# Optimization experiments

Hardware: AMD Instinct MI355X
Metric: run time of the kernel (lower is better)

## Reference

```python
import jax, jax.numpy as jnp
import numpy as np

N_NODES = 100000
N_DIM = 128   # node feature dim
L10 = 128
L11 = 128     # dim_hop0 == L11 (required by Spatial_Attention_0 einsum)
B = 2048      # batch of target nodes
S1 = 10       # hop-1 fanout
S2 = 25       # hop-2 fanout per hop-1 neighbor


def setup_inputs() -> dict:
    key = jax.random.key(0)
    ks = jax.random.split(key, 9)
    tn = lambda k, shape: jax.random.truncated_normal(k, -2.0, 2.0, shape, jnp.float32) * 0.1 - 0.1
    return {
        "x": jax.random.normal(ks[0], (N_NODES, N_DIM), jnp.float32),
        "samples": jax.random.randint(ks[1], (B, 1 + S1 + S1 * S2), 0, N_NODES),
        "V1_h1_att": tn(ks[2], (L11, N_DIM)),
        "w1_h1": tn(ks[3], (2 * L11,)),
        "V1_h0_att": tn(ks[4], (L10, L11)),
        "w1_h0": tn(ks[5], (2 * L10,)),
        "V1_h1": tn(ks[6], (L11, N_DIM)),
        "V1_h0": tn(ks[7], (L10, L11)),
        "W_hops": tn(ks[8], (L11, 2 * L11)),
    }


def _att1(feat, V, w):
    # feat: [..., s, 2*n]; project both halves with V [L, n], score with w [2L],
    # leaky_relu then softmax over the neighbor axis (axis -2 of feat).
    n = V.shape[1]
    L = V.shape[0]
    t1 = jnp.einsum('...sn,ln->...sl', feat[..., :n], V)
    t2 = jnp.einsum('...sn,ln->...sl', feat[..., n:], V)
    logits = jnp.einsum('l,...sl->...s', w[:L], t1) + jnp.einsum('l,...sl->...s', w[L:], t2)
    return jax.nn.softmax(jax.nn.leaky_relu(logits), axis=-1)


def reference(x, samples, V1_h1_att, w1_h1, V1_h0_att, w1_h0, V1_h1, V1_h0, W_hops):
    s1, s2 = S1, S2
    idx2 = samples[:, -(s1 * s2):].reshape(-1, s1, s2)   # hop-2 neighbor ids [B,s1,s2]
    idx1 = samples[:, 1:1 + s1]                          # hop-1 neighbor ids [B,s1]
    idx0 = samples[:, 0]                                 # targets [B]

    # ---- hop-1 aggregation (attention over the s2 hop-2 neighbors) ----
    fea_n2 = x[idx2]                                     # [B,s1,s2,n] irregular gather
    fea_t1 = x[idx1]                                     # [B,s1,n]
    fea_tar2 = jnp.concatenate(
        [jnp.broadcast_to(fea_t1[:, :, None, :], fea_n2.shape), fea_n2], axis=-1)
    beta1 = _att1(fea_tar2, V1_h1_att, w1_h1)            # [B,s1,s2]
    emb_n2 = jnp.einsum('bstn,ln->bstl', fea_n2, V1_h1)  # [B,s1,s2,L11]
    agg1 = jnp.einsum('bst,bstl->bsl', beta1, emb_n2)    # [B,s1,L11]
    emb_t1 = jnp.einsum('bsn,ln->bsl', fea_t1, V1_h1)    # [B,s1,L11]
    hop1 = jax.nn.sigmoid(
        jnp.einsum('dj,bsj->bsd', W_hops, jnp.concatenate([emb_t1, agg1], -1)))  # [B,s1,L11]

    # ---- hop-0 aggregation (attention over the s1 hop-1 neighbors) ----
    fea_t0 = x[idx0]                                     # [B,n]
    fea_tar1 = jnp.concatenate(
        [jnp.broadcast_to(fea_t0[:, None, :], fea_t1.shape), fea_t1], axis=-1)
    beta0 = _att1(fea_tar1, V1_h1_att, w1_h1)            # [B,s1]
    agg0 = jnp.einsum('bs,bsl->bl', beta0, emb_t1)       # emb of hop-1 nbrs == emb_t1
    emb_t0 = fea_t0 @ V1_h1.T                            # [B,L11]
    hop0 = jax.nn.sigmoid(jnp.concatenate([emb_t0, agg0], -1) @ W_hops.T)  # [B,L11]

    # ---- combine hops with Spatial_Attention_0 ----
    t1c = jnp.einsum('bd,ld->bl', hop0, V1_h0_att)       # target proj (tiled over s1)
    t2c = jnp.einsum('bsd,ld->bsl', hop1, V1_h0_att)     # [B,s1,L10]
    logits = (jnp.einsum('l,bl->b', w1_h0[:L10], t1c)[:, None]
              + jnp.einsum('l,bsl->bs', w1_h0[L10:], t2c))
    beta_h = jax.nn.softmax(jax.nn.leaky_relu(logits), axis=1)  # [B,s1]
    emb_h1 = jnp.einsum('bsd,ld->bsl', hop1, V1_h0)      # [B,s1,L10]
    fea_out = jnp.einsum('bs,bsl->bl', beta_h, emb_h1)   # [B,L10]

    beta_step = jnp.concatenate([beta_h[:, :, None], beta1], axis=2)  # [B,s1,1+s2]
    return fea_out.T, beta_step
```

## Files before the change

kernel.cpp:

```cpp
#include <hip/hip_runtime.h>
#include <math.h>

#define S1C 10
#define S2C 25
#define DC 128
#define NSAMP 261
#define NBATCH 2048
#define FEA_SZ (128*2048)

#define WS_BPK   512
#define WS_V0T   (WS_BPK + 16384)
#define WS_AGGF  (WS_V0T + 16384)

typedef float f32x4 __attribute__((ext_vector_type(4)));
typedef short s16x8 __attribute__((ext_vector_type(8)));

__device__ __forceinline__ float lrelu(float v) { return v > 0.f ? v : 0.01f * v; }
__device__ __forceinline__ float sigm(float v) { return 1.f / (1.f + __expf(-v)); }
__device__ __forceinline__ float dot4(float4 a, float4 b) {
    return a.x * b.x + a.y * b.y + a.z * b.z + a.w * b.w;
}
__device__ __forceinline__ unsigned short f2bf(float f) {
    unsigned u = __float_as_uint(f);
    unsigned r = (u + 0x7FFFu + ((u >> 16) & 1u)) >> 16;
    return (unsigned short)r;
}

__global__ void prep_all_kernel(const float* __restrict__ Vh1a, const float* __restrict__ w1,
                                const float* __restrict__ Vh0a, const float* __restrict__ w0,
                                const float* __restrict__ V1h1, const float* __restrict__ Whops,
                                const float* __restrict__ V1h0, float* __restrict__ ws) {
    const int blk = blockIdx.x, tid = threadIdx.x;
    if (blk == 0) {
        for (int o = tid; o < 512; o += 256) {
            int which = o >> 7, n = o & 127;
            const float* V = (which < 2) ? Vh1a : Vh0a;
            const float* w = (which < 2) ? w1 : w0;
            int off = (which & 1) * 128;
            float acc = 0.f;
            for (int l = 0; l < 128; ++l) acc += V[l * 128 + n] * w[off + l];
            ws[o] = acc;
        }
    } else if (blk <= 128) {
        int e = (blk - 1) * 256 + tid;
        int j  = e & 7;
        int l  = (e >> 3) & 63;
        int kb = (e >> 9) & 7;
        int nt = (e >> 12) & 7;
        int d  = nt * 16 + (l & 15);
        int k  = kb * 32 + ((l >> 4) & 3) * 8 + j;
        int which = k >> 7, kk = k & 127;
        float acc = 0.f;
        for (int jj = 0; jj < 128; ++jj)
            acc += Whops[(size_t)d * 256 + which * 128 + jj] * V1h1[(size_t)jj * 128 + kk];
        unsigned short* bpk = (unsigned short*)(ws + WS_BPK);
        bpk[e] = f2bf(acc);
    } else {
        int dd = (blk - 129) * 2 + (tid >> 7);
        int l = tid & 127;
        ws[WS_V0T + (size_t)dd * 128 + l] = V1h0[(size_t)l * 128 + dd];
    }
}

__global__ __launch_bounds__(256) void nbr_kernel(
    const float* __restrict__ x, const int* __restrict__ samples,
    const float* __restrict__ ws, unsigned short* __restrict__ aggF,
    float* __restrict__ out)
{
    const int s = blockIdx.x, b = blockIdx.y;
    const int tid = threadIdx.x, g = tid >> 5, lane = tid & 31;

    __shared__ __align__(16) float sNbr[25][132];
    __shared__ float sD[26];
    __shared__ float sBeta[25];

    float4 a1v = *(const float4*)(ws + lane * 4);
    float4 a2v = *(const float4*)(ws + 128 + lane * 4);
    const int* sidx = samples + (size_t)b * NSAMP;

    const bool has3 = (g < 2);
    int n0 = sidx[11 + s * S2C + g];
    int n1 = sidx[11 + s * S2C + 8 + g];
    int n2 = sidx[11 + s * S2C + 16 + g];
    int n3 = has3 ? ((g == 0) ? sidx[11 + s * S2C + 24] : sidx[1 + s]) : 0;

    float4 v0 = *(const float4*)(x + (size_t)n0 * DC + lane * 4);
    float4 v1 = *(const float4*)(x + (size_t)n1 * DC + lane * 4);
    float4 v2 = *(const float4*)(x + (size_t)n2 * DC + lane * 4);
    float4 v3 = make_float4(0.f, 0.f, 0.f, 0.f);
    if (has3) v3 = *(const float4*)(x + (size_t)n3 * DC + lane * 4);

    *(float4*)(&sNbr[g][lane * 4]) = v0;
    *(float4*)(&sNbr[8 + g][lane * 4]) = v1;
    *(float4*)(&sNbr[16 + g][lane * 4]) = v2;
    if (g == 0) *(float4*)(&sNbr[24][lane * 4]) = v3;

    float p0 = dot4(v0, a2v);
    float p1 = dot4(v1, a2v);
    float p2 = dot4(v2, a2v);
    float p3 = has3 ? dot4(v3, (g == 0) ? a2v : a1v) : 0.f;
    #pragma unroll
    for (int o = 16; o > 0; o >>= 1) {
        p0 += __shfl_xor(p0, o, 32);
        p1 += __shfl_xor(p1, o, 32);
        p2 += __shfl_xor(p2, o, 32);
        p3 += __shfl_xor(p3, o, 32);
    }
    if (lane == 0) {
        sD[g] = p0; sD[8 + g] = p1; sD[16 + g] = p2;
        if (has3) sD[24 + g] = p3;
    }
    __syncthreads();

    if (tid < 32) {
        float c1 = sD[25];
        float v = (lane < 25) ? lrelu(c1 + sD[lane]) : -3.4e38f;
        float m = v;
        for (int o = 16; o > 0; o >>= 1) m = fmaxf(m, __shfl_xor(m, o, 32));
        float e = (lane < 25) ? __expf(v - m) : 0.f;
        float ssum = e;
        for (int o = 16; o > 0; o >>= 1) ssum += __shfl_xor(ssum, o, 32);
        if (lane < 25) {
            float bt = e / ssum;
            sBeta[lane] = bt;
            out[FEA_SZ + (size_t)b * 260 + s * 26 + 1 + lane] = bt;
        }
    }
    __syncthreads();

    if (tid < 128) {
        float acc = 0.f;
        #pragma unroll
        for (int t = 0; t < 25; ++t) acc += sBeta[t] * sNbr[t][tid];
        aggF[((size_t)b * 10 + s) * 128 + tid] = f2bf(acc);
    }
}

__global__ __launch_bounds__(256, 4) void hopfused_kernel(
    const float* __restrict__ x, const int* __restrict__ samples,
    const float* __restrict__ ws, const unsigned short* __restrict__ aggF,
    float* __restrict__ out)
{
    const int b0 = blockIdx.x * 2;
    const int tid = threadIdx.x;
    const int w = tid >> 6;
    const int lane = tid & 63;
    const int lg16 = lane >> 4;
    const int l15 = lane & 15;

    __shared__ __align__(16) float sX[22][128];
    __shared__ __align__(16) short sXb[32][264];
    __shared__ float sLgP[4][32];
    __shared__ __align__(16) float sHopH[2][128];
    __shared__ float sD[22];
    __shared__ float sBeta0[2][10];
    __shared__ float sBH[2][10];
    __shared__ int sNode[22];

    if (tid < 22) {
        int bb = tid / 11, s = tid - bb * 11;
        sNode[tid] = (s < 10) ? samples[(size_t)(b0 + bb) * NSAMP + 1 + s]
                              : samples[(size_t)(b0 + bb) * NSAMP];
    }
    for (int i = tid; i < 330; i += 256) {
        int rr = i / 33, c8 = i - rr * 33;
        int row = (rr < 5) ? 11 + rr : 22 + rr;
        s16x8 z = (s16x8)(short)0;
        *(s16x8*)(&sXb[row][c8 * 8]) = z;
    }
    __syncthreads();

    for (int i = tid; i < 22 * 32; i += 256) {
        int row = i >> 5, seg = i & 31;
        *(float4*)(&sX[row][seg * 4]) =
            *(const float4*)(x + (size_t)sNode[row] * DC + seg * 4);
    }
    for (int i = tid; i < 320; i += 256) {
        int row20 = i >> 4, seg = i & 15;
        int bb = row20 / 10, s = row20 - bb * 10;
        *(s16x8*)(&sXb[bb * 16 + s][128 + seg * 8]) =
            *(const s16x8*)(aggF + ((size_t)(b0 + bb) * 10 + s) * 128 + seg * 8);
    }
    __syncthreads();

    {
        int gg = tid >> 5, ln = tid & 31;
        for (int rd = 0, r = gg; rd < 3; ++rd, r += 8) {
            float p = 0.f;
            if (r < 22) {
                int s = (r < 11) ? r : r - 11;
                const float* av = ws + ((s < 10) ? 128 : 0);
                float4 v = *(const float4*)(&sX[r][ln * 4]);
                float4 a = *(const float4*)(av + ln * 4);
                p = dot4(v, a);
            }
            for (int o = 16; o > 0; o >>= 1) p += __shfl_xor(p, o, 32);
            if (r < 22 && ln == 0) sD[r] = p;
        }
    }
    __syncthreads();

    if (tid < 32) {
        int bb = tid >> 4, j = tid & 15;
        float cc = sD[bb * 11 + 10];
        float v = (j < 10) ? lrelu(cc + sD[bb * 11 + j]) : -3.4e38f;
        float m = v;
        for (int o = 8; o > 0; o >>= 1) m = fmaxf(m, __shfl_xor(m, o, 16));
        float e = (j < 10) ? __expf(v - m) : 0.f;
        float ss = e;
        for (int o = 8; o > 0; o >>= 1) ss += __shfl_xor(ss, o, 16);
        if (j < 10) sBeta0[bb][j] = e / ss;
    }
    __syncthreads();

    {
        int bb = tid >> 7, n = tid & 127;
        float acc = 0.f;
        #pragma unroll
        for (int s = 0; s < 10; ++s) acc += sBeta0[bb][s] * sX[bb * 11 + s][n];
        sXb[bb * 16 + 10][128 + n] = (short)f2bf(acc);
    }
    for (int i = tid; i < 22 * 128; i += 256) {
        int m = i >> 7, k = i & 127;
        int row = (m < 11) ? m : m + 5;
        sXb[row][k] = (short)f2bf(sX[m][k]);
    }
    __syncthreads();

    const unsigned short* bpk = (const unsigned short*)(ws + WS_BPK);
    const int nt0 = 2 * w, nt1 = nt0 + 1;
    f32x4 acc00 = {0.f, 0.f, 0.f, 0.f}, acc01 = {0.f, 0.f, 0.f, 0.f};
    f32x4 acc10 = {0.f, 0.f, 0.f, 0.f}, acc11 = {0.f, 0.f, 0.f, 0.f};
    #pragma unroll
    for (int kb = 0; kb < 8; ++kb) {
        s16x8 a0 = *(const s16x8*)(&sXb[l15][kb * 32 + lg16 * 8]);
        s16x8 a1 = *(const s16x8*)(&sXb[16 + l15][kb * 32 + lg16 * 8]);
        s16x8 bw0 = *(const s16x8*)(bpk + ((size_t)(nt0 * 8 + kb) * 64 + lane) * 8);
        s16x8 bw1 = *(const s16x8*)(bpk + ((size_t)(nt1 * 8 + kb) * 64 + lane) * 8);
        acc00 = __builtin_amdgcn_mfma_f32_16x16x32_bf16(a0, bw0, acc00, 0, 0, 0);
        acc01 = __builtin_amdgcn_mfma_f32_16x16x32_bf16(a0, bw1, acc01, 0, 0, 0);
        acc10 = __builtin_amdgcn_mfma_f32_16x16x32_bf16(a1, bw0, acc10, 0, 0, 0);
        acc11 = __builtin_amdgcn_mfma_f32_16x16x32_bf16(a1, bw1, acc11, 0, 0, 0);
    }

    float h00[4], h01[4], h10[4], h11[4];
    #pragma unroll
    for (int r = 0; r < 4; ++r) {
        h00[r] = sigm(acc00[r]); h01[r] = sigm(acc01[r]);
        h10[r] = sigm(acc10[r]); h11[r] = sigm(acc11[r]);
    }

    const int c0 = nt0 * 16 + l15, c1 = nt1 * 16 + l15;
    const float b1c0 = ws[256 + c0], b1c1 = ws[256 + c1];
    const float b2c0 = ws[384 + c0], b2c1 = ws[384 + c1];
    #pragma unroll
    for (int mt = 0; mt < 2; ++mt) {
        #pragma unroll
        for (int r = 0; r < 4; ++r) {
            int s = lg16 * 4 + r;
            float ha = mt ? h10[r] : h00[r];
            float hb = mt ? h11[r] : h01[r];
            float p;
            if (s < 10)       p = ha * b2c0 + hb * b2c1;
            else if (s == 10) p = ha * b1c0 + hb * b1c1;
            else              p = 0.f;
            #pragma unroll
            for (int o = 1; o < 16; o <<= 1) p += __shfl_xor(p, o, 64);
            if (l15 == 0) sLgP[w][mt * 16 + s] = p;
        }
    }
    __syncthreads();

    if (tid < 32) {
        int bb = tid >> 4, j = tid & 15;
        float lgj = 0.f, lg10 = 0.f;
        #pragma unroll
        for (int wv = 0; wv < 4; ++wv) {
            lgj  += sLgP[wv][bb * 16 + j];
            lg10 += sLgP[wv][bb * 16 + 10];
        }
        float v = (j < 10) ? lrelu(lg10 + lgj) : -3.4e38f;
        float m = v;
        for (int o = 8; o > 0; o >>= 1) m = fmaxf(m, __shfl_xor(m, o, 16));
        float e = (j < 10) ? __expf(v - m) : 0.f;
        float ss = e;
        for (int o = 8; o > 0; o >>= 1) ss += __shfl_xor(ss, o, 16);
        if (j < 10) {
            float bh = e / ss;
            sBH[bb][j] = bh;
            out[FEA_SZ + (size_t)(b0 + bb) * 260 + j * 26] = bh;
        }
    }
    __syncthreads();

    #pragma unroll
    for (int bb = 0; bb < 2; ++bb) {
        float p0 = 0.f, p1 = 0.f;
        #pragma unroll
        for (int r = 0; r < 4; ++r) {
            int s = lg16 * 4 + r;
            if (s < 10) {
                float bh = sBH[bb][s];
                p0 += bh * (bb ? h10[r] : h00[r]);
                p1 += bh * (bb ? h11[r] : h01[r]);
            }
        }
        p0 += __shfl_xor(p0, 16, 64); p0 += __shfl_xor(p0, 32, 64);
        p1 += __shfl_xor(p1, 16, 64); p1 += __shfl_xor(p1, 32, 64);
        if (lg16 == 0) {
            sHopH[bb][nt0 * 16 + l15] = p0;
            sHopH[bb][nt1 * 16 + l15] = p1;
        }
    }
    __syncthreads();

    {
        const float* v0t = ws + WS_V0T;
        int c = tid & 127, bb = tid >> 7;
        float acc2 = 0.f;
        for (int dd = 0; dd < 128; dd += 4) {
            float4 hh = *(const float4*)(&sHopH[bb][dd]);
            acc2 += hh.x * v0t[(size_t)(dd + 0) * 128 + c]
                  + hh.y * v0t[(size_t)(dd + 1) * 128 + c]
                  + hh.z * v0t[(size_t)(dd + 2) * 128 + c]
                  + hh.w * v0t[(size_t)(dd + 3) * 128 + c];
        }
        out[(size_t)c * 2048 + b0 + bb] = acc2;
    }
}

extern "C" void kernel_launch(void* const* d_in, const int* in_sizes, int n_in,
                              void* d_out, int out_size, void* d_ws, size_t ws_size,
                              hipStream_t stream) {
    const float* x      = (const float*)d_in[0];
    const int*   samples= (const int*)d_in[1];
    const float* V1h1a  = (const float*)d_in[2];
    const float* w1h1   = (const float*)d_in[3];
    const float* V1h0a  = (const float*)d_in[4];
    const float* w1h0   = (const float*)d_in[5];
    const float* V1h1   = (const float*)d_in[6];
    const float* V1h0   = (const float*)d_in[7];
    const float* Whops  = (const float*)d_in[8];
    float* outp = (float*)d_out;
    float* ws   = (float*)d_ws;
    unsigned short* aggF = (unsigned short*)(ws + WS_AGGF);

    hipLaunchKernelGGL(prep_all_kernel, dim3(193), dim3(256), 0, stream,
                       V1h1a, w1h1, V1h0a, w1h0, V1h1, Whops, V1h0, ws);
    hipLaunchKernelGGL(nbr_kernel, dim3(10, 2048), dim3(256), 0, stream,
                       x, samples, ws, aggF, outp);
    hipLaunchKernelGGL(hopfused_kernel, dim3(1024), dim3(256), 0, stream,
                       x, samples, ws, aggF, outp);
}
```

Before: 71.79 us.

## Convert node features to bf16 once per call and gather bf16 rows

Adds a pass in the prep kernel that converts the full feature table to bf16 in workspace. New neighbor and hop kernels then gather bf16 rows instead of fp32, halving the bytes of the irregular gathers. In exchange it streams the whole table each call and loses precision in the attention inputs. The new path is enabled only when the workspace is large enough.

```diff
diff --git a/kernel.cpp b/kernel.cpp
--- a/kernel.cpp
+++ b/kernel.cpp
@@ -6,14 +6,18 @@
 #define DC 128
 #define NSAMP 261
 #define NBATCH 2048
+#define N_NODES 100000
 #define FEA_SZ (128*2048)
 
 #define WS_BPK   512
 #define WS_V0T   (WS_BPK + 16384)
 #define WS_AGGF  (WS_V0T + 16384)
+#define WS_XB    (WS_AGGF + 1310720)
+#define WS_END   (WS_XB + 6400000)
 
 typedef float f32x4 __attribute__((ext_vector_type(4)));
 typedef short s16x8 __attribute__((ext_vector_type(8)));
+typedef short s16x4 __attribute__((ext_vector_type(4)));
 
 __device__ __forceinline__ float lrelu(float v) { return v > 0.f ? v : 0.01f * v; }
 __device__ __forceinline__ float sigm(float v) { return 1.f / (1.f + __expf(-v)); }
@@ -25,11 +29,15 @@
     unsigned r = (u + 0x7FFFu + ((u >> 16) & 1u)) >> 16;
     return (unsigned short)r;
 }
+__device__ __forceinline__ float bf2f(unsigned short us) {
+    return __uint_as_float(((unsigned)us) << 16);
+}
 
 __global__ void prep_all_kernel(const float* __restrict__ Vh1a, const float* __restrict__ w1,
                                 const float* __restrict__ Vh0a, const float* __restrict__ w0,
                                 const float* __restrict__ V1h1, const float* __restrict__ Whops,
-                                const float* __restrict__ V1h0, float* __restrict__ ws) {
+                                const float* __restrict__ V1h0, const float* __restrict__ x,
+                                unsigned short* __restrict__ xb, float* __restrict__ ws) {
     const int blk = blockIdx.x, tid = threadIdx.x;
     if (blk == 0) {
         for (int o = tid; o < 512; o += 256) {
@@ -55,12 +63,289 @@
             acc += Whops[(size_t)d * 256 + which * 128 + jj] * V1h1[(size_t)jj * 128 + kk];
         unsigned short* bpk = (unsigned short*)(ws + WS_BPK);
         bpk[e] = f2bf(acc);
-    } else {
+    } else if (blk <= 192) {
         int dd = (blk - 129) * 2 + (tid >> 7);
         int l = tid & 127;
         ws[WS_V0T + (size_t)dd * 128 + l] = V1h0[(size_t)l * 128 + dd];
-    }
-}
+    } else {
+        const int total4 = N_NODES * DC / 4;
+        const int stride = (gridDim.x - 193) * 256;
+        const float4* x4 = (const float4*)x;
+        for (int i = (blk - 193) * 256 + tid; i < total4; i += stride) {
+            float4 v = x4[i];
+            s16x4 o;
+            o[0] = (short)f2bf(v.x); o[1] = (short)f2bf(v.y);
+            o[2] = (short)f2bf(v.z); o[3] = (short)f2bf(v.w);
+            *(s16x4*)(xb + (size_t)i * 4) = o;
+        }
+    }
+}
+
+
+__global__ __launch_bounds__(256) void nbr_b_kernel(
+    const unsigned short* __restrict__ xb, const int* __restrict__ samples,
+    const float* __restrict__ ws, unsigned short* __restrict__ aggF,
+    float* __restrict__ out)
+{
+    const int s = blockIdx.x, b = blockIdx.y;
+    const int tid = threadIdx.x, g = tid >> 5, lane = tid & 31;
+
+    __shared__ __align__(16) unsigned short sNbr[25][136];
+    __shared__ float sD[26];
+    __shared__ float sBeta[25];
+
+    float4 a1v = *(const float4*)(ws + lane * 4);
+    float4 a2v = *(const float4*)(ws + 128 + lane * 4);
+    const int* sidx = samples + (size_t)b * NSAMP;
+
+    const bool has3 = (g < 2);
+    int n0 = sidx[11 + s * S2C + g];
+    int n1 = sidx[11 + s * S2C + 8 + g];
+    int n2 = sidx[11 + s * S2C + 16 + g];
+    int n3 = has3 ? ((g == 0) ? sidx[11 + s * S2C + 24] : sidx[1 + s]) : 0;
+
+    s16x4 v0 = *(const s16x4*)(xb + (size_t)n0 * DC + lane * 4);
+    s16x4 v1 = *(const s16x4*)(xb + (size_t)n1 * DC + lane * 4);
+    s16x4 v2 = *(const s16x4*)(xb + (size_t)n2 * DC + lane * 4);
+    s16x4 v3 = (s16x4)(short)0;
+    if (has3) v3 = *(const s16x4*)(xb + (size_t)n3 * DC + lane * 4);
+
+    *(s16x4*)(&sNbr[g][lane * 4]) = v0;
+    *(s16x4*)(&sNbr[8 + g][lane * 4]) = v1;
+    *(s16x4*)(&sNbr[16 + g][lane * 4]) = v2;
+    if (g == 0) *(s16x4*)(&sNbr[24][lane * 4]) = v3;
+
+    float p0 = bf2f((unsigned short)v0[0]) * a2v.x + bf2f((unsigned short)v0[1]) * a2v.y
+             + bf2f((unsigned short)v0[2]) * a2v.z + bf2f((unsigned short)v0[3]) * a2v.w;
+    float p1 = bf2f((unsigned short)v1[0]) * a2v.x + bf2f((unsigned short)v1[1]) * a2v.y
+             + bf2f((unsigned short)v1[2]) * a2v.z + bf2f((unsigned short)v1[3]) * a2v.w;
+    float p2 = bf2f((unsigned short)v2[0]) * a2v.x + bf2f((unsigned short)v2[1]) * a2v.y
+             + bf2f((unsigned short)v2[2]) * a2v.z + bf2f((unsigned short)v2[3]) * a2v.w;
+    float4 av3 = (g == 0) ? a2v : a1v;
+    float p3 = has3 ? (bf2f((unsigned short)v3[0]) * av3.x + bf2f((unsigned short)v3[1]) * av3.y
+                     + bf2f((unsigned short)v3[2]) * av3.z + bf2f((unsigned short)v3[3]) * av3.w) : 0.f;
+    #pragma unroll
+    for (int o = 16; o > 0; o >>= 1) {
+        p0 += __shfl_xor(p0, o, 32);
+        p1 += __shfl_xor(p1, o, 32);
+        p2 += __shfl_xor(p2, o, 32);
+        p3 += __shfl_xor(p3, o, 32);
+    }
+    if (lane == 0) {
+        sD[g] = p0; sD[8 + g] = p1; sD[16 + g] = p2;
+        if (has3) sD[24 + g] = p3;
+    }
+    __syncthreads();
+
+    if (tid < 32) {
+        float c1 = sD[25];
+        float v = (lane < 25) ? lrelu(c1 + sD[lane]) : -3.4e38f;
+        float m = v;
+        for (int o = 16; o > 0; o >>= 1) m = fmaxf(m, __shfl_xor(m, o, 32));
+        float e = (lane < 25) ? __expf(v - m) : 0.f;
+        float ssum = e;
+        for (int o = 16; o > 0; o >>= 1) ssum += __shfl_xor(ssum, o, 32);
+        if (lane < 25) {
+            float bt = e / ssum;
+            sBeta[lane] = bt;
+            out[FEA_SZ + (size_t)b * 260 + s * 26 + 1 + lane] = bt;
+        }
+    }
+    __syncthreads();
+
+    if (tid < 128) {
+        float acc = 0.f;
+        #pragma unroll
+        for (int t = 0; t < 25; ++t) acc += sBeta[t] * bf2f(sNbr[t][tid]);
+        aggF[((size_t)b * 10 + s) * 128 + tid] = f2bf(acc);
+    }
+}
+
+__global__ __launch_bounds__(256, 4) void hopfused_b_kernel(
+    const unsigned short* __restrict__ xb, const int* __restrict__ samples,
+    const float* __restrict__ ws, const unsigned short* __restrict__ aggF,
+    float* __restrict__ out)
+{
+    const int b0 = blockIdx.x * 2;
+    const int tid = threadIdx.x;
+    const int w = tid >> 6;
+    const int lane = tid & 63;
+    const int lg16 = lane >> 4;
+    const int l15 = lane & 15;
+
+    __shared__ __align__(16) short sXb[32][264];
+    __shared__ float sLgP[4][32];
+    __shared__ __align__(16) float sHopH[2][128];
+    __shared__ float sD[22];
+    __shared__ float sBeta0[2][10];
+    __shared__ float sBH[2][10];
+    __shared__ int sNode[22];
+
+    if (tid < 22) {
+        int bb = tid / 11, s = tid - bb * 11;
+        sNode[tid] = (s < 10) ? samples[(size_t)(b0 + bb) * NSAMP + 1 + s]
+                              : samples[(size_t)(b0 + bb) * NSAMP];
+    }
+    for (int i = tid; i < 330; i += 256) {
+        int rr = i / 33, c8 = i - rr * 33;
+        int row = (rr < 5) ? 11 + rr : 22 + rr;
+        s16x8 z = (s16x8)(short)0;
+        *(s16x8*)(&sXb[row][c8 * 8]) = z;
+    }
+    __syncthreads();
+
+    for (int it = 0; it < 2; ++it) {
+        int i = it * 256 + tid;
+        if (i < 22 * 16) {
+            int r = i >> 4, seg = i & 15;
+            int bb = r / 11, s = r - bb * 11;
+            s16x8 v = *(const s16x8*)(xb + (size_t)sNode[r] * DC + seg * 8);
+            *(s16x8*)(&sXb[bb * 16 + s][seg * 8]) = v;
+            const float* av = ws + ((s < 10) ? 128 : 0);
+            float4 a0 = *(const float4*)(av + seg * 8);
+            float4 a1 = *(const float4*)(av + seg * 8 + 4);
+            float p = bf2f((unsigned short)v[0]) * a0.x + bf2f((unsigned short)v[1]) * a0.y
+                    + bf2f((unsigned short)v[2]) * a0.z + bf2f((unsigned short)v[3]) * a0.w
+                    + bf2f((unsigned short)v[4]) * a1.x + bf2f((unsigned short)v[5]) * a1.y
+                    + bf2f((unsigned short)v[6]) * a1.z + bf2f((unsigned short)v[7]) * a1.w;
+            #pragma unroll
+            for (int o = 8; o > 0; o >>= 1) p += __shfl_xor(p, o, 16);
+            if (seg == 0) sD[r] = p;
+        }
+    }
+    for (int i = tid; i < 320; i += 256) {
+        int row20 = i >> 4, seg = i & 15;
+        int bb = row20 / 10, s = row20 - bb * 10;
+        *(s16x8*)(&sXb[bb * 16 + s][128 + seg * 8]) =
+            *(const s16x8*)(aggF + ((size_t)(b0 + bb) * 10 + s) * 128 + seg * 8);
+    }
+    __syncthreads();
+
+    if (tid < 32) {
+        int bb = tid >> 4, j = tid & 15;
+        float cc = sD[bb * 11 + 10];
+        float v = (j < 10) ? lrelu(cc + sD[bb * 11 + j]) : -3.4e38f;
+        float m = v;
+        for (int o = 8; o > 0; o >>= 1) m = fmaxf(m, __shfl_xor(m, o, 16));
+        float e = (j < 10) ? __expf(v - m) : 0.f;
+        float ss = e;
+        for (int o = 8; o > 0; o >>= 1) ss += __shfl_xor(ss, o, 16);
+        if (j < 10) sBeta0[bb][j] = e / ss;
+    }
+    __syncthreads();
+
+    {
+        int bb = tid >> 7, n = tid & 127;
+        float acc = 0.f;
+        #pragma unroll
+        for (int s = 0; s < 10; ++s)
+            acc += sBeta0[bb][s] * bf2f((unsigned short)sXb[bb * 16 + s][n]);
+        sXb[bb * 16 + 10][128 + n] = (short)f2bf(acc);
+    }
+    __syncthreads();
+
+    const unsigned short* bpk = (const unsigned short*)(ws + WS_BPK);
+    const int nt0 = 2 * w, nt1 = nt0 + 1;
+    f32x4 acc00 = {0.f, 0.f, 0.f, 0.f}, acc01 = {0.f, 0.f, 0.f, 0.f};
+    f32x4 acc10 = {0.f, 0.f, 0.f, 0.f}, acc11 = {0.f, 0.f, 0.f, 0.f};
+    #pragma unroll
+    for (int kb = 0; kb < 8; ++kb) {
+        s16x8 a0 = *(const s16x8*)(&sXb[l15][kb * 32 + lg16 * 8]);
+        s16x8 a1 = *(const s16x8*)(&sXb[16 + l15][kb * 32 + lg16 * 8]);
+        s16x8 bw0 = *(const s16x8*)(bpk + ((size_t)(nt0 * 8 + kb) * 64 + lane) * 8);
+        s16x8 bw1 = *(const s16x8*)(bpk + ((size_t)(nt1 * 8 + kb) * 64 + lane) * 8);
+        acc00 = __builtin_amdgcn_mfma_f32_16x16x32_bf16(a0, bw0, acc00, 0, 0, 0);
+        acc01 = __builtin_amdgcn_mfma_f32_16x16x32_bf16(a0, bw1, acc01, 0, 0, 0);
+        acc10 = __builtin_amdgcn_mfma_f32_16x16x32_bf16(a1, bw0, acc10, 0, 0, 0);
+        acc11 = __builtin_amdgcn_mfma_f32_16x16x32_bf16(a1, bw1, acc11, 0, 0, 0);
+    }
+
+    float h00[4], h01[4], h10[4], h11[4];
+    #pragma unroll
+    for (int r = 0; r < 4; ++r) {
+        h00[r] = sigm(acc00[r]); h01[r] = sigm(acc01[r]);
+        h10[r] = sigm(acc10[r]); h11[r] = sigm(acc11[r]);
+    }
+
+    const int c0 = nt0 * 16 + l15, c1 = nt1 * 16 + l15;
+    const float b1c0 = ws[256 + c0], b1c1 = ws[256 + c1];
+    const float b2c0 = ws[384 + c0], b2c1 = ws[384 + c1];
+    #pragma unroll
+    for (int mt = 0; mt < 2; ++mt) {
+        #pragma unroll
+        for (int r = 0; r < 4; ++r) {
+            int s = lg16 * 4 + r;
+            float ha = mt ? h10[r] : h00[r];
+            float hb = mt ? h11[r] : h01[r];
+            float p;
+            if (s < 10)       p = ha * b2c0 + hb * b2c1;
+            else if (s == 10) p = ha * b1c0 + hb * b1c1;
+            else              p = 0.f;
+            #pragma unroll
+            for (int o = 1; o < 16; o <<= 1) p += __shfl_xor(p, o, 64);
+            if (l15 == 0) sLgP[w][mt * 16 + s] = p;
+        }
+    }
+    __syncthreads();
+
+    if (tid < 32) {
+        int bb = tid >> 4, j = tid & 15;
+        float lgj = 0.f, lg10 = 0.f;
+        #pragma unroll
+        for (int wv = 0; wv < 4; ++wv) {
+            lgj  += sLgP[wv][bb * 16 + j];
+            lg10 += sLgP[wv][bb * 16 + 10];
+        }
+        float v = (j < 10) ? lrelu(lg10 + lgj) : -3.4e38f;
+        float m = v;
+        for (int o = 8; o > 0; o >>= 1) m = fmaxf(m, __shfl_xor(m, o, 16));
+        float e = (j < 10) ? __expf(v - m) : 0.f;
+        float ss = e;
+        for (int o = 8; o > 0; o >>= 1) ss += __shfl_xor(ss, o, 16);
+        if (j < 10) {
+            float bh = e / ss;
+            sBH[bb][j] = bh;
+            out[FEA_SZ + (size_t)(b0 + bb) * 260 + j * 26] = bh;
+        }
+    }
+    __syncthreads();
+
+    #pragma unroll
+    for (int bb = 0; bb < 2; ++bb) {
+        float p0 = 0.f, p1 = 0.f;
+        #pragma unroll
+        for (int r = 0; r < 4; ++r) {
+            int s = lg16 * 4 + r;
+            if (s < 10) {
+                float bh = sBH[bb][s];
+                p0 += bh * (bb ? h10[r] : h00[r]);
+                p1 += bh * (bb ? h11[r] : h01[r]);
+            }
+        }
+        p0 += __shfl_xor(p0, 16, 64); p0 += __shfl_xor(p0, 32, 64);
+        p1 += __shfl_xor(p1, 16, 64); p1 += __shfl_xor(p1, 32, 64);
+        if (lg16 == 0) {
+            sHopH[bb][nt0 * 16 + l15] = p0;
+            sHopH[bb][nt1 * 16 + l15] = p1;
+        }
+    }
+    __syncthreads();
+
+    {
+        const float* v0t = ws + WS_V0T;
+        int c = tid & 127, bb = tid >> 7;
+        float acc2 = 0.f;
+        for (int dd = 0; dd < 128; dd += 4) {
+            float4 hh = *(const float4*)(&sHopH[bb][dd]);
+            acc2 += hh.x * v0t[(size_t)(dd + 0) * 128 + c]
+                  + hh.y * v0t[(size_t)(dd + 1) * 128 + c]
+                  + hh.z * v0t[(size_t)(dd + 2) * 128 + c]
+                  + hh.w * v0t[(size_t)(dd + 3) * 128 + c];
+        }
+        out[(size_t)c * 2048 + b0 + bb] = acc2;
+    }
+}
+
 
 __global__ __launch_bounds__(256) void nbr_kernel(
     const float* __restrict__ x, const int* __restrict__ samples,
@@ -344,11 +629,23 @@
     float* outp = (float*)d_out;
     float* ws   = (float*)d_ws;
     unsigned short* aggF = (unsigned short*)(ws + WS_AGGF);
-
-    hipLaunchKernelGGL(prep_all_kernel, dim3(193), dim3(256), 0, stream,
-                       V1h1a, w1h1, V1h0a, w1h0, V1h1, Whops, V1h0, ws);
-    hipLaunchKernelGGL(nbr_kernel, dim3(10, 2048), dim3(256), 0, stream,
-                       x, samples, ws, aggF, outp);
-    hipLaunchKernelGGL(hopfused_kernel, dim3(1024), dim3(256), 0, stream,
-                       x, samples, ws, aggF, outp);
-}
+    unsigned short* xb   = (unsigned short*)(ws + WS_XB);
+
+    const bool use_bf16x = ws_size >= (size_t)WS_END * sizeof(float);
+
+    if (use_bf16x) {
+        hipLaunchKernelGGL(prep_all_kernel, dim3(193 + 2048), dim3(256), 0, stream,
+                           V1h1a, w1h1, V1h0a, w1h0, V1h1, Whops, V1h0, x, xb, ws);
+        hipLaunchKernelGGL(nbr_b_kernel, dim3(10, 2048), dim3(256), 0, stream,
+                           xb, samples, ws, aggF, outp);
+        hipLaunchKernelGGL(hopfused_b_kernel, dim3(1024), dim3(256), 0, stream,
+                           xb, samples, ws, aggF, outp);
+    } else {
+        hipLaunchKernelGGL(prep_all_kernel, dim3(193), dim3(256), 0, stream,
+                           V1h1a, w1h1, V1h0a, w1h0, V1h1, Whops, V1h0, x, (unsigned short*)nullptr, ws);
+        hipLaunchKernelGGL(nbr_kernel, dim3(10, 2048), dim3(256), 0, stream,
+                           x, samples, ws, aggF, outp);
+        hipLaunchKernelGGL(hopfused_kernel, dim3(1024), dim3(256), 0, stream,
+                           x, samples, ws, aggF, outp);
+    }
+}
```

After: 71.91 us. No clear change (+0.2%).
